# Performance work log

Hardware: AMD Instinct MI355X
Metric: run time of the kernel (lower is better)

## Reference

```python
import jax, jax.numpy as jnp
import numpy as np

N = 50000
E = 1600000
IN = 128
HID = 128
OUT = 64
NEG_SLOPE = 0.2  # DGL GATConv default leaky_relu slope


def _gat_layer(h, src, dst, W, al, ar, b, res=None, act=True):
    """DGL GATConv layer on an edge-list graph.
    h: [N, F_in]; W: [F_in, H*D]; al, ar, b: [H, D]; res: None | [N,H,D].
    Returns [N, H, D].
    """
    H, D = al.shape
    f = (h @ W).reshape(N, H, D)                      # fc projection
    el = jnp.sum(f * al, axis=-1)                     # [N, H]
    er = jnp.sum(f * ar, axis=-1)                     # [N, H]
    e = jax.nn.leaky_relu(el[src] + er[dst], NEG_SLOPE)  # [E, H]
    # edge softmax over incoming edges of each dst node
    m = jax.ops.segment_max(e, dst, num_segments=N)   # [N, H]
    ex = jnp.exp(e - m[dst])                          # [E, H]
    s = jax.ops.segment_sum(ex, dst, num_segments=N)  # [N, H]
    alpha = ex / s[dst]                               # [E, H]
    msg = f[src] * alpha[..., None]                   # [E, H, D]
    rst = jax.ops.segment_sum(msg, dst, num_segments=N)  # [N, H, D]
    if res is not None:
        rst = rst + res
    rst = rst + b                                     # bias [H, D] broadcast
    if act:
        rst = jax.nn.elu(rst)
    return rst


def setup_inputs() -> dict:
    key = jax.random.key(0)
    ks = jax.random.split(key, 16)
    x = jax.random.normal(ks[0], (N, IN), dtype=jnp.float32)
    src = jax.random.randint(ks[1], (E,), 0, N)
    dst = jax.random.randint(ks[2], (E,), 0, N)
    sc = 0.05
    # layer 0: IN -> 8 heads x 16, no residual, elu
    W0 = jax.random.normal(ks[3], (IN, 8 * 16), dtype=jnp.float32) * sc
    al0 = jax.random.normal(ks[4], (8, 16), dtype=jnp.float32) * sc
    ar0 = jax.random.normal(ks[5], (8, 16), dtype=jnp.float32) * sc
    b0 = jnp.zeros((8, 16), dtype=jnp.float32)
    # layer 1: HID -> 8 heads x 16, identity residual (HID == 8*16), elu
    W1 = jax.random.normal(ks[6], (HID, 8 * 16), dtype=jnp.float32) * sc
    al1 = jax.random.normal(ks[7], (8, 16), dtype=jnp.float32) * sc
    ar1 = jax.random.normal(ks[8], (8, 16), dtype=jnp.float32) * sc
    b1 = jnp.zeros((8, 16), dtype=jnp.float32)
    # layer 2: HID -> 1 head x 64, linear residual (128 != 64), no act
    W2 = jax.random.normal(ks[9], (HID, 1 * OUT), dtype=jnp.float32) * sc
    al2 = jax.random.normal(ks[10], (1, OUT), dtype=jnp.float32) * sc
    ar2 = jax.random.normal(ks[11], (1, OUT), dtype=jnp.float32) * sc
    b2 = jnp.zeros((1, OUT), dtype=jnp.float32)
    resW2 = jax.random.normal(ks[12], (HID, 1 * OUT), dtype=jnp.float32) * sc
    return {"x": x, "src": src, "dst": dst,
            "W0": W0, "al0": al0, "ar0": ar0, "b0": b0,
            "W1": W1, "al1": al1, "ar1": ar1, "b1": b1,
            "W2": W2, "al2": al2, "ar2": ar2, "b2": b2,
            "resW2": resW2}


def reference(x, src, dst, W0, al0, ar0, b0, W1, al1, ar1, b1,
              W2, al2, ar2, b2, resW2):
    # layer 0: no residual, elu, flatten heads (dropout=0)
    h = _gat_layer(x, src, dst, W0, al0, ar0, b0, res=None, act=True)
    h = h.reshape(N, -1)  # [N, 128]
    # layer 1: identity residual, elu, flatten heads
    res1 = h.reshape(N, 8, 16)
    h = _gat_layer(h, src, dst, W1, al1, ar1, b1, res=res1, act=True)
    h = h.reshape(N, -1)  # [N, 128]
    # layer 2: linear residual, no activation, mean over heads
    res2 = (h @ resW2).reshape(N, 1, OUT)
    h = _gat_layer(h, src, dst, W2, al2, ar2, b2, res=res2, act=False)
    return h.mean(axis=1)  # [N, 64]
```

## Files before the change

kernel.cpp:

```cpp
#include <hip/hip_runtime.h>
#include <hip/hip_fp16.h>
#include <math.h>


#define GN 50000
#define GE 1600000
#define NB 391
#define NBLK_A 512
#define CHUNK 3125
#define NBD 200
#define DCH 250

typedef _Float16 half8 __attribute__((ext_vector_type(8)));
typedef _Float16 half4v __attribute__((ext_vector_type(4)));
typedef float f32x4 __attribute__((ext_vector_type(4)));


__global__ __launch_bounds__(256) void bucketA(const int* __restrict__ dst, int* __restrict__ cnt) {
    __shared__ int hist[NB];
    for (int i = threadIdx.x; i < NB; i += 256) hist[i] = 0;
    __syncthreads();
    int b = blockIdx.x;
    int beg = b * CHUNK, end = beg + CHUNK;
    for (int i = beg + threadIdx.x; i < end; i += 256)
        atomicAdd(&hist[dst[i] >> 7], 1);
    __syncthreads();
    for (int k = threadIdx.x; k < NB; k += 256)
        cnt[k * NBLK_A + b] = hist[k];
}

__global__ __launch_bounds__(512) void bucketB(int* __restrict__ cnt, int* __restrict__ tot) {
    __shared__ int s[512];
    int k = blockIdx.x, t = threadIdx.x;
    int* row = cnt + k * NBLK_A;
    s[t] = row[t];
    __syncthreads();
    for (int ofs = 1; ofs < 512; ofs <<= 1) {
        int v = (t >= ofs) ? s[t - ofs] : 0;
        __syncthreads();
        s[t] += v;
        __syncthreads();
    }
    row[t] = (t == 0) ? 0 : s[t - 1];
    if (t == 511) tot[k] = s[511];
}

__global__ __launch_bounds__(512) void bucketB2(const int* __restrict__ tot, int* __restrict__ base,
                                                int* __restrict__ offs) {
    __shared__ int s[512];
    int t = threadIdx.x;
    s[t] = (t < NB) ? tot[t] : 0;
    __syncthreads();
    for (int ofs = 1; ofs < 512; ofs <<= 1) {
        int v = (t >= ofs) ? s[t - ofs] : 0;
        __syncthreads();
        s[t] += v;
        __syncthreads();
    }
    if (t <= NB) base[t] = (t == 0) ? 0 : s[t - 1];
    if (t == 0) offs[GN] = GE;
}

__global__ __launch_bounds__(256) void bucketC(const int* __restrict__ src, const int* __restrict__ dst,
                                               const int* __restrict__ cnt, const int* __restrict__ base,
                                               unsigned* __restrict__ ebuf) {
    __shared__ int cur[NB];
    int b = blockIdx.x;
    for (int k = threadIdx.x; k < NB; k += 256)
        cur[k] = base[k] + cnt[k * NBLK_A + b];
    __syncthreads();
    int beg = b * CHUNK, end = beg + CHUNK;
    for (int i = beg + threadIdx.x; i < end; i += 256) {
        int d = dst[i];
        int pos = atomicAdd(&cur[d >> 7], 1);
        ebuf[pos] = (unsigned)src[i] | ((unsigned)(d & 127) << 16);
    }
}

__global__ __launch_bounds__(256) void bucketD(const unsigned* __restrict__ ebuf, const int* __restrict__ base,
                                               int* __restrict__ offs, unsigned short* __restrict__ csrc) {
    __shared__ int hist[4096];
    __shared__ int psum[256];
    int k = blockIdx.x, t = threadIdx.x;
    #pragma unroll
    for (int i = 0; i < 16; ++i) hist[t * 16 + i] = 0;
    __syncthreads();
    int lo = base[k], hi = base[k + 1];
    for (int i = lo + t; i < hi; i += 256) {
        unsigned v = ebuf[i];
        unsigned key = ((v >> 16) << 5) | ((v & 0xFFFFu) >> 11);
        atomicAdd(&hist[key], 1);
    }
    __syncthreads();
    int loc[16];
    int s = 0;
    #pragma unroll
    for (int i = 0; i < 16; ++i) { loc[i] = s; s += hist[t * 16 + i]; }
    psum[t] = s;
    __syncthreads();
    for (int ofs = 1; ofs < 256; ofs <<= 1) {
        int v = (t >= ofs) ? psum[t - ofs] : 0;
        __syncthreads();
        psum[t] += v;
        __syncthreads();
    }
    int basek = lo + ((t == 0) ? 0 : psum[t - 1]);
    #pragma unroll
    for (int i = 0; i < 16; ++i) hist[t * 16 + i] = basek + loc[i];
    __syncthreads();
    if (t < 128) {
        int node = (k << 7) + t;
        if (node < GN) offs[node] = hist[t * 32];
    }
    __syncthreads();
    for (int i = lo + t; i < hi; i += 256) {
        unsigned v = ebuf[i];
        unsigned key = ((v >> 16) << 5) | ((v & 0xFFFFu) >> 11);
        int pos = atomicAdd(&hist[key], 1);
        csrc[pos] = (unsigned short)(v & 0xFFFFu);
    }
}


__global__ __launch_bounds__(256) void dhist(const int* __restrict__ offs, int* __restrict__ dcnt) {
    __shared__ int hist[128];
    int b = blockIdx.x, t = threadIdx.x;
    if (t < 128) hist[t] = 0;
    __syncthreads();
    int n = b * DCH + t;
    if (t < DCH && n < GN) {
        int d = offs[n + 1] - offs[n];
        d = (d > 127) ? 127 : d;
        atomicAdd(&hist[d], 1);
    }
    __syncthreads();
    if (t < 128) dcnt[t * NBD + b] = hist[t];
}

__global__ __launch_bounds__(256) void dscanB(int* __restrict__ dcnt, int* __restrict__ dtot) {
    __shared__ int s[256];
    int k = blockIdx.x, t = threadIdx.x;
    int* row = dcnt + k * NBD;
    s[t] = (t < NBD) ? row[t] : 0;
    __syncthreads();
    for (int ofs = 1; ofs < 256; ofs <<= 1) {
        int v = (t >= ofs) ? s[t - ofs] : 0;
        __syncthreads();
        s[t] += v;
        __syncthreads();
    }
    if (t < NBD) row[t] = (t == 0) ? 0 : s[t - 1];
    if (t == 255) dtot[k] = s[255];
}

__global__ __launch_bounds__(128) void dscanB2(const int* __restrict__ dtot, int* __restrict__ dbase) {
    __shared__ int s[128];
    int t = threadIdx.x;
    s[t] = dtot[t];
    __syncthreads();
    for (int ofs = 1; ofs < 128; ofs <<= 1) {
        int v = (t >= ofs) ? s[t - ofs] : 0;
        __syncthreads();
        s[t] += v;
        __syncthreads();
    }
    dbase[t] = (t == 0) ? 0 : s[t - 1];
}

__global__ __launch_bounds__(256) void dscat(const int* __restrict__ offs, const int* __restrict__ dcnt,
                                             const int* __restrict__ dbase, int* __restrict__ perm) {
    __shared__ int cur[128];
    int b = blockIdx.x, t = threadIdx.x;
    if (t < 128) cur[t] = dbase[t] + dcnt[t * NBD + b];
    __syncthreads();
    int n = b * DCH + t;
    if (t < DCH && n < GN) {
        int d = offs[n + 1] - offs[n];
        d = (d > 127) ? 127 : d;
        int pos = atomicAdd(&cur[d], 1);
        perm[pos] = n;
    }
}


__global__ __launch_bounds__(256) void prep(const float* __restrict__ W0, const float* __restrict__ W1,
                                            const float* __restrict__ W2, const float* __restrict__ rW2,
                                            const float* __restrict__ al0, const float* __restrict__ ar0,
                                            const float* __restrict__ al1, const float* __restrict__ ar1,
                                            const float* __restrict__ al2, const float* __restrict__ ar2,
                                            _Float16* __restrict__ w0t, _Float16* __restrict__ w1t,
                                            _Float16* __restrict__ w2t, _Float16* __restrict__ rw2t,
                                            _Float16* __restrict__ aB0, _Float16* __restrict__ aB1,
                                            _Float16* __restrict__ aB2) {
    int i = blockIdx.x * 256 + threadIdx.x;
    if (i < 16384) {
        int n = i >> 7, k = i & 127;
        w0t[i] = (_Float16)W0[k * 128 + n];
        w1t[i] = (_Float16)W1[k * 128 + n];
    }
    if (i < 8192) {
        int n = i >> 7, k = i & 127;
        w2t[i] = (_Float16)W2[k * 64 + n];
        rw2t[i] = (_Float16)rW2[k * 64 + n];
    }
    if (i < 2048) {
        int n = i >> 7, k = i & 127;
        _Float16 v0 = (_Float16)0.f, v1 = (_Float16)0.f, v2 = (_Float16)0.f;
        if (n < 8) {
            if ((k >> 4) == n) {
                v0 = (_Float16)al0[n * 16 + (k & 15)];
                v1 = (_Float16)al1[n * 16 + (k & 15)];
            }
        } else {
            int h = n - 8;
            if ((k >> 4) == h) {
                v0 = (_Float16)ar0[h * 16 + (k & 15)];
                v1 = (_Float16)ar1[h * 16 + (k & 15)];
            }
        }
        if (n == 0 && k < 64) v2 = (_Float16)al2[k];
        if (n == 1 && k < 64) v2 = (_Float16)ar2[k];
        aB0[i] = v0; aB1[i] = v1; aB2[i] = v2;
    }
}


template <int NT, bool AF32, bool DUAL, bool MULTI>
__global__ __launch_bounds__(256) void gemm_att(const void* __restrict__ Av,
                                                const _Float16* __restrict__ WT,
                                                const _Float16* __restrict__ WT2,
                                                const _Float16* __restrict__ attB,
                                                _Float16* __restrict__ C, _Float16* __restrict__ C2,
                                                float* __restrict__ elb, float* __restrict__ erb,
                                                int nrows) {
    const int N = NT * 16;
    __shared__ _Float16 lt[4][16][NT * 16 + 4];
    int wave = threadIdx.x >> 6, lane = threadIdx.x & 63;
    int quad = lane >> 4, l16 = lane & 15;
    int m = blockIdx.x * 64 + wave * 16 + l16;
    int mc = (m < nrows) ? m : (nrows - 1);
    half8 a[4];
    if (AF32) {
        const float* ap = (const float*)Av + (size_t)mc * 128 + quad * 8;
        #pragma unroll
        for (int kk = 0; kk < 4; ++kk) {
            float4 u = *(const float4*)(ap + kk * 32);
            float4 v = *(const float4*)(ap + kk * 32 + 4);
            half8 t;
            t[0] = (_Float16)u.x; t[1] = (_Float16)u.y; t[2] = (_Float16)u.z; t[3] = (_Float16)u.w;
            t[4] = (_Float16)v.x; t[5] = (_Float16)v.y; t[6] = (_Float16)v.z; t[7] = (_Float16)v.w;
            a[kk] = t;
        }
    } else {
        const _Float16* ap = (const _Float16*)Av + (size_t)mc * 128 + quad * 8;
        #pragma unroll
        for (int kk = 0; kk < 4; ++kk) a[kk] = *(const half8*)(ap + kk * 32);
    }
    f32x4 acc[NT];
    f32x4 acc2[DUAL ? NT : 1];
    #pragma unroll
    for (int nt = 0; nt < NT; ++nt) acc[nt] = (f32x4){0.f, 0.f, 0.f, 0.f};
    if (DUAL) {
        #pragma unroll
        for (int nt = 0; nt < NT; ++nt) acc2[nt] = (f32x4){0.f, 0.f, 0.f, 0.f};
    }
    const _Float16* wp = WT + (size_t)l16 * 128 + quad * 8;
    const _Float16* wp2 = DUAL ? (WT2 + (size_t)l16 * 128 + quad * 8) : WT;
    #pragma unroll
    for (int nt = 0; nt < NT; ++nt) {
        #pragma unroll
        for (int kk = 0; kk < 4; ++kk) {
            half8 b = *(const half8*)(wp + nt * 16 * 128 + kk * 32);
            acc[nt] = __builtin_amdgcn_mfma_f32_16x16x32_f16(a[kk], b, acc[nt], 0, 0, 0);
            if (DUAL) {
                half8 b2 = *(const half8*)(wp2 + nt * 16 * 128 + kk * 32);
                acc2[nt] = __builtin_amdgcn_mfma_f32_16x16x32_f16(a[kk], b2, acc2[nt], 0, 0, 0);
            }
        }
    }
    int row0 = blockIdx.x * 64 + wave * 16 + quad * 4;
    #pragma unroll
    for (int nt = 0; nt < NT; ++nt) {
        #pragma unroll
        for (int r = 0; r < 4; ++r) {
            _Float16 hv = (_Float16)acc[nt][r];
            lt[wave][quad * 4 + r][nt * 16 + l16] = hv;
            int row = row0 + r;
            if (row < nrows) {
                C[(size_t)row * N + nt * 16 + l16] = hv;
                if (DUAL) C2[(size_t)row * N + nt * 16 + l16] = (_Float16)acc2[nt][r];
            }
        }
    }
    f32x4 att = {0.f, 0.f, 0.f, 0.f};
    const _Float16* bp = attB + (size_t)l16 * 128 + quad * 8;
    constexpr int KCH = (NT == 8) ? 4 : 2;
    #pragma unroll
    for (int kk = 0; kk < KCH; ++kk) {
        const _Float16* lp = &lt[wave][l16][kk * 32 + quad * 8];
        half4v lo = *(const half4v*)lp;
        half4v hi = *(const half4v*)(lp + 4);
        half8 af = __builtin_shufflevector(lo, hi, 0, 1, 2, 3, 4, 5, 6, 7);
        half8 bf = *(const half8*)(bp + kk * 32);
        att = __builtin_amdgcn_mfma_f32_16x16x32_f16(af, bf, att, 0, 0, 0);
    }
    if (MULTI) {
        int hh = l16 & 7;
        float* dstp = (l16 < 8) ? elb : erb;
        #pragma unroll
        for (int r = 0; r < 4; ++r) {
            int row = row0 + r;
            if (row < nrows) dstp[row * 8 + hh] = att[r];
        }
    } else {
        if (l16 < 2) {
            float* dstp = (l16 == 0) ? elb : erb;
            #pragma unroll
            for (int r = 0; r < 4; ++r) {
                int row = row0 + r;
                if (row < nrows) dstp[row] = att[r];
            }
        }
    }
}


__global__ __launch_bounds__(256) void agg_multi(const int* __restrict__ offs,
                                                 const unsigned short* __restrict__ csrc,
                                                 const int* __restrict__ perm,
                                                 const _Float16* __restrict__ fh, const float* __restrict__ el,
                                                 const float* __restrict__ er, const float* __restrict__ bias,
                                                 const _Float16* __restrict__ resid, _Float16* __restrict__ out,
                                                 int n) {
    int slot = blockIdx.x * 16 + (threadIdx.x >> 4);
    int lg = threadIdx.x & 15;
    if (slot >= n) return;
    int node = perm[n - 1 - slot];
    int head = lg >> 1;
    float ern = er[node * 8 + head];
    int beg = offs[node], end = offs[node + 1];
    float acc[8] = {};
    float ssum = 0.f;
    int e = beg;
    for (; e + 4 <= end; e += 4) {
        int s0 = csrc[e], s1 = csrc[e + 1], s2 = csrc[e + 2], s3 = csrc[e + 3];
        float e0 = el[s0 * 8 + head] + ern;
        float e1 = el[s1 * 8 + head] + ern;
        float e2 = el[s2 * 8 + head] + ern;
        float e3 = el[s3 * 8 + head] + ern;
        half8 q0 = *(const half8*)(fh + (size_t)s0 * 128 + lg * 8);
        half8 q1 = *(const half8*)(fh + (size_t)s1 * 128 + lg * 8);
        half8 q2 = *(const half8*)(fh + (size_t)s2 * 128 + lg * 8);
        half8 q3 = *(const half8*)(fh + (size_t)s3 * 128 + lg * 8);
        e0 = fmaxf(e0, 0.2f * e0);
        e1 = fmaxf(e1, 0.2f * e1);
        e2 = fmaxf(e2, 0.2f * e2);
        e3 = fmaxf(e3, 0.2f * e3);
        float w0 = __expf(e0), w1 = __expf(e1), w2 = __expf(e2), w3 = __expf(e3);
        ssum += (w0 + w1) + (w2 + w3);
        #pragma unroll
        for (int i = 0; i < 8; ++i)
            acc[i] += w0 * (float)q0[i] + w1 * (float)q1[i]
                    + w2 * (float)q2[i] + w3 * (float)q3[i];
    }
    for (; e < end; ++e) {
        int s = csrc[e];
        float ev = el[s * 8 + head] + ern;
        ev = fmaxf(ev, 0.2f * ev);
        float w = __expf(ev);
        half8 q = *(const half8*)(fh + (size_t)s * 128 + lg * 8);
        ssum += w;
        #pragma unroll
        for (int i = 0; i < 8; ++i) acc[i] += w * (float)q[i];
    }
    float inv = (ssum > 0.f) ? 1.0f / ssum : 0.f;
    float o[8];
    #pragma unroll
    for (int j = 0; j < 8; ++j) o[j] = acc[j] * inv + bias[lg * 8 + j];
    if (resid) {
        half8 r = *(const half8*)(resid + (size_t)node * 128 + lg * 8);
        #pragma unroll
        for (int j = 0; j < 8; ++j) o[j] += (float)r[j];
    }
    half8 ov;
    #pragma unroll
    for (int j = 0; j < 8; ++j) {
        float v = o[j];
        v = (v > 0.f) ? v : expm1f(v);
        ov[j] = (_Float16)v;
    }
    *(half8*)(out + (size_t)node * 128 + lg * 8) = ov;
}

__global__ __launch_bounds__(256) void agg_single(const int* __restrict__ offs,
                                                  const unsigned short* __restrict__ csrc,
                                                  const int* __restrict__ perm,
                                                  const _Float16* __restrict__ fh, const float* __restrict__ el,
                                                  const float* __restrict__ er, const float* __restrict__ bias,
                                                  const _Float16* __restrict__ resid, float* __restrict__ out,
                                                  int n) {
    int slot = blockIdx.x * 16 + (threadIdx.x >> 4);
    int lg = threadIdx.x & 15;
    if (slot >= n) return;
    int node = perm[n - 1 - slot];
    float ern = er[node];
    int beg = offs[node], end = offs[node + 1];
    float acc[4] = {};
    float ssum = 0.f;
    int e = beg;
    for (; e + 4 <= end; e += 4) {
        int s0 = csrc[e], s1 = csrc[e + 1], s2 = csrc[e + 2], s3 = csrc[e + 3];
        float e0 = el[s0] + ern;
        float e1 = el[s1] + ern;
        float e2 = el[s2] + ern;
        float e3 = el[s3] + ern;
        half4v q0 = *(const half4v*)(fh + (size_t)s0 * 64 + lg * 4);
        half4v q1 = *(const half4v*)(fh + (size_t)s1 * 64 + lg * 4);
        half4v q2 = *(const half4v*)(fh + (size_t)s2 * 64 + lg * 4);
        half4v q3 = *(const half4v*)(fh + (size_t)s3 * 64 + lg * 4);
        e0 = fmaxf(e0, 0.2f * e0);
        e1 = fmaxf(e1, 0.2f * e1);
        e2 = fmaxf(e2, 0.2f * e2);
        e3 = fmaxf(e3, 0.2f * e3);
        float w0 = __expf(e0), w1 = __expf(e1), w2 = __expf(e2), w3 = __expf(e3);
        ssum += (w0 + w1) + (w2 + w3);
        #pragma unroll
        for (int i = 0; i < 4; ++i)
            acc[i] += w0 * (float)q0[i] + w1 * (float)q1[i]
                    + w2 * (float)q2[i] + w3 * (float)q3[i];
    }
    for (; e < end; ++e) {
        int s = csrc[e];
        float ev = el[s] + ern;
        ev = fmaxf(ev, 0.2f * ev);
        float w = __expf(ev);
        half4v q = *(const half4v*)(fh + (size_t)s * 64 + lg * 4);
        ssum += w;
        #pragma unroll
        for (int i = 0; i < 4; ++i) acc[i] += w * (float)q[i];
    }
    float inv = (ssum > 0.f) ? 1.0f / ssum : 0.f;
    half4v r = *(const half4v*)(resid + (size_t)node * 64 + lg * 4);
    float4 o;
    o.x = acc[0] * inv + bias[lg * 4 + 0] + (float)r[0];
    o.y = acc[1] * inv + bias[lg * 4 + 1] + (float)r[1];
    o.z = acc[2] * inv + bias[lg * 4 + 2] + (float)r[2];
    o.w = acc[3] * inv + bias[lg * 4 + 3] + (float)r[3];
    *(float4*)(out + (size_t)node * 64 + lg * 4) = o;
}


extern "C" void kernel_launch(void* const* d_in, const int* in_sizes, int n_in,
                              void* d_out, int out_size, void* d_ws, size_t ws_size,
                              hipStream_t stream) {
    const float* x     = (const float*)d_in[0];
    const int*   src   = (const int*)d_in[1];
    const int*   dst   = (const int*)d_in[2];
    const float* W0    = (const float*)d_in[3];
    const float* al0   = (const float*)d_in[4];
    const float* ar0   = (const float*)d_in[5];
    const float* b0    = (const float*)d_in[6];
    const float* W1    = (const float*)d_in[7];
    const float* al1   = (const float*)d_in[8];
    const float* ar1   = (const float*)d_in[9];
    const float* b1    = (const float*)d_in[10];
    const float* W2    = (const float*)d_in[11];
    const float* al2   = (const float*)d_in[12];
    const float* ar2   = (const float*)d_in[13];
    const float* b2    = (const float*)d_in[14];
    const float* resW2 = (const float*)d_in[15];
    float* out = (float*)d_out;

    char* w = (char*)d_ws;
    auto alloc = [&](size_t bytes) {
        char* p = w;
        w += (bytes + 255) & ~(size_t)255;
        return p;
    };
    int*            base  = (int*)alloc((size_t)(NB + 1) * 4);
    int*            offs  = (int*)alloc((size_t)(GN + 1) * 4);
    unsigned short* csrc  = (unsigned short*)alloc((size_t)GE * 2);
    int*            perm  = (int*)alloc((size_t)GN * 4);
    int*            dcnt  = (int*)alloc((size_t)128 * NBD * 4);
    int*            dtot  = (int*)alloc(128 * 4);
    int*            dbase = (int*)alloc(128 * 4);
    _Float16*       fbuf  = (_Float16*)alloc((size_t)GN * 128 * 2);
    float*          elb   = (float*)alloc((size_t)GN * 8 * 4);
    float*          erb   = (float*)alloc((size_t)GN * 8 * 4);
    _Float16*       hA    = (_Float16*)alloc((size_t)GN * 128 * 2);
    _Float16*       hB    = (_Float16*)alloc((size_t)GN * 128 * 2);
    _Float16*       res2  = (_Float16*)alloc((size_t)GN * 64 * 2);
    _Float16*       w0t   = (_Float16*)alloc(128 * 128 * 2);
    _Float16*       w1t   = (_Float16*)alloc(128 * 128 * 2);
    _Float16*       w2t   = (_Float16*)alloc(64 * 128 * 2);
    _Float16*       rw2t  = (_Float16*)alloc(64 * 128 * 2);
    _Float16*       aB0   = (_Float16*)alloc(16 * 128 * 2);
    _Float16*       aB1   = (_Float16*)alloc(16 * 128 * 2);
    _Float16*       aB2   = (_Float16*)alloc(16 * 128 * 2);

    int*      cnt  = (int*)hA;
    int*      tot  = (int*)hA + NB * NBLK_A;
    unsigned* ebuf = (unsigned*)hB;

    bucketA<<<NBLK_A, 256, 0, stream>>>(dst, cnt);
    bucketB<<<NB, 512, 0, stream>>>(cnt, tot);
    bucketB2<<<1, 512, 0, stream>>>(tot, base, offs);
    bucketC<<<NBLK_A, 256, 0, stream>>>(src, dst, cnt, base, ebuf);
    bucketD<<<NB, 256, 0, stream>>>(ebuf, base, offs, csrc);

    dhist<<<NBD, 256, 0, stream>>>(offs, dcnt);
    dscanB<<<128, 256, 0, stream>>>(dcnt, dtot);
    dscanB2<<<1, 128, 0, stream>>>(dtot, dbase);
    dscat<<<NBD, 256, 0, stream>>>(offs, dcnt, dbase, perm);

    prep<<<64, 256, 0, stream>>>(W0, W1, W2, resW2, al0, ar0, al1, ar1, al2, ar2,
                                 w0t, w1t, w2t, rw2t, aB0, aB1, aB2);

    dim3 gblk(256);
    int gemmGrid = (GN + 63) / 64;
    int aggGrid = (GN + 15) / 16;

    gemm_att<8, true, false, true><<<gemmGrid, gblk, 0, stream>>>(
        x, w0t, nullptr, aB0, fbuf, nullptr, elb, erb, GN);
    agg_multi<<<aggGrid, gblk, 0, stream>>>(offs, csrc, perm, fbuf, elb, erb, b0, nullptr, hA, GN);

    gemm_att<8, false, false, true><<<gemmGrid, gblk, 0, stream>>>(
        hA, w1t, nullptr, aB1, fbuf, nullptr, elb, erb, GN);
    agg_multi<<<aggGrid, gblk, 0, stream>>>(offs, csrc, perm, fbuf, elb, erb, b1, hA, hB, GN);

    gemm_att<4, false, true, false><<<gemmGrid, gblk, 0, stream>>>(
        hB, w2t, rw2t, aB2, fbuf, res2, elb, erb, GN);
    agg_single<<<aggGrid, gblk, 0, stream>>>(offs, csrc, perm, fbuf, elb, erb, b2, res2, out, GN);
}
```

Before: 358.6 us.

## Fuse degree histogram into CSR build and store attention logits in fp16

Computes the per-node degree histogram inside bucketD with global atomics, replacing the dhist/dscanB/dscanB2 chain. The small scan is merged into the weight-prep kernel, and the scatter now uses global atomics. The el/er attention logits are stored as fp16 instead of fp32, halving their footprint for the gather in the aggregation kernels. This cuts several launches and some memory traffic, at the cost of global atomic contention on 128 counters and reduced precision in the logits.

```diff
diff --git a/kernel.cpp b/kernel.cpp
--- a/kernel.cpp
+++ b/kernel.cpp
@@ -8,15 +8,15 @@
 #define NB 391
 #define NBLK_A 512
 #define CHUNK 3125
-#define NBD 200
-#define DCH 250
 
 typedef _Float16 half8 __attribute__((ext_vector_type(8)));
 typedef _Float16 half4v __attribute__((ext_vector_type(4)));
 typedef float f32x4 __attribute__((ext_vector_type(4)));
 
 
-__global__ __launch_bounds__(256) void bucketA(const int* __restrict__ dst, int* __restrict__ cnt) {
+__global__ __launch_bounds__(256) void bucketA(const int* __restrict__ dst, int* __restrict__ cnt,
+                                               int* __restrict__ gdcnt) {
+    if (blockIdx.x == 0 && threadIdx.x < 128) gdcnt[threadIdx.x] = 0;
     __shared__ int hist[NB];
     for (int i = threadIdx.x; i < NB; i += 256) hist[i] = 0;
     __syncthreads();
@@ -78,7 +78,8 @@
 }
 
 __global__ __launch_bounds__(256) void bucketD(const unsigned* __restrict__ ebuf, const int* __restrict__ base,
-                                               int* __restrict__ offs, unsigned short* __restrict__ csrc) {
+                                               int* __restrict__ offs, unsigned short* __restrict__ csrc,
+                                               int* __restrict__ gdcnt) {
     __shared__ int hist[4096];
     __shared__ int psum[256];
     int k = blockIdx.x, t = threadIdx.x;
@@ -110,7 +111,14 @@
     __syncthreads();
     if (t < 128) {
         int node = (k << 7) + t;
-        if (node < GN) offs[node] = hist[t * 32];
+        if (node < GN) {
+            int st = hist[t * 32];
+            offs[node] = st;
+            int en = (t < 127) ? hist[(t + 1) * 32] : hi;
+            int d = en - st;
+            d = (d > 127) ? 127 : d;
+            atomicAdd(&gdcnt[d], 1);
+        }
     }
     __syncthreads();
     for (int i = lo + t; i < hi; i += 256) {
@@ -122,78 +130,33 @@
 }
 
 
-__global__ __launch_bounds__(256) void dhist(const int* __restrict__ offs, int* __restrict__ dcnt) {
-    __shared__ int hist[128];
-    int b = blockIdx.x, t = threadIdx.x;
-    if (t < 128) hist[t] = 0;
-    __syncthreads();
-    int n = b * DCH + t;
-    if (t < DCH && n < GN) {
-        int d = offs[n + 1] - offs[n];
-        d = (d > 127) ? 127 : d;
-        atomicAdd(&hist[d], 1);
-    }
-    __syncthreads();
-    if (t < 128) dcnt[t * NBD + b] = hist[t];
-}
-
-__global__ __launch_bounds__(256) void dscanB(int* __restrict__ dcnt, int* __restrict__ dtot) {
-    __shared__ int s[256];
-    int k = blockIdx.x, t = threadIdx.x;
-    int* row = dcnt + k * NBD;
-    s[t] = (t < NBD) ? row[t] : 0;
-    __syncthreads();
-    for (int ofs = 1; ofs < 256; ofs <<= 1) {
-        int v = (t >= ofs) ? s[t - ofs] : 0;
-        __syncthreads();
-        s[t] += v;
-        __syncthreads();
-    }
-    if (t < NBD) row[t] = (t == 0) ? 0 : s[t - 1];
-    if (t == 255) dtot[k] = s[255];
-}
-
-__global__ __launch_bounds__(128) void dscanB2(const int* __restrict__ dtot, int* __restrict__ dbase) {
-    __shared__ int s[128];
-    int t = threadIdx.x;
-    s[t] = dtot[t];
-    __syncthreads();
-    for (int ofs = 1; ofs < 128; ofs <<= 1) {
-        int v = (t >= ofs) ? s[t - ofs] : 0;
-        __syncthreads();
-        s[t] += v;
-        __syncthreads();
-    }
-    dbase[t] = (t == 0) ? 0 : s[t - 1];
-}
-
-__global__ __launch_bounds__(256) void dscat(const int* __restrict__ offs, const int* __restrict__ dcnt,
-                                             const int* __restrict__ dbase, int* __restrict__ perm) {
-    __shared__ int cur[128];
-    int b = blockIdx.x, t = threadIdx.x;
-    if (t < 128) cur[t] = dbase[t] + dcnt[t * NBD + b];
-    __syncthreads();
-    int n = b * DCH + t;
-    if (t < DCH && n < GN) {
-        int d = offs[n + 1] - offs[n];
-        d = (d > 127) ? 127 : d;
-        int pos = atomicAdd(&cur[d], 1);
-        perm[pos] = n;
-    }
-}
-
-
-__global__ __launch_bounds__(256) void prep(const float* __restrict__ W0, const float* __restrict__ W1,
-                                            const float* __restrict__ W2, const float* __restrict__ rW2,
-                                            const float* __restrict__ al0, const float* __restrict__ ar0,
-                                            const float* __restrict__ al1, const float* __restrict__ ar1,
-                                            const float* __restrict__ al2, const float* __restrict__ ar2,
-                                            _Float16* __restrict__ w0t, _Float16* __restrict__ w1t,
-                                            _Float16* __restrict__ w2t, _Float16* __restrict__ rw2t,
-                                            _Float16* __restrict__ aB0, _Float16* __restrict__ aB1,
-                                            _Float16* __restrict__ aB2) {
-    int i = blockIdx.x * 256 + threadIdx.x;
-    if (i < 16384) {
+__global__ __launch_bounds__(256) void dscan_prep(const int* __restrict__ gdcnt, int* __restrict__ gcur,
+                                                  const float* __restrict__ W0, const float* __restrict__ W1,
+                                                  const float* __restrict__ W2, const float* __restrict__ rW2,
+                                                  const float* __restrict__ al0, const float* __restrict__ ar0,
+                                                  const float* __restrict__ al1, const float* __restrict__ ar1,
+                                                  const float* __restrict__ al2, const float* __restrict__ ar2,
+                                                  _Float16* __restrict__ w0t, _Float16* __restrict__ w1t,
+                                                  _Float16* __restrict__ w2t, _Float16* __restrict__ rw2t,
+                                                  _Float16* __restrict__ aB0, _Float16* __restrict__ aB1,
+                                                  _Float16* __restrict__ aB2) {
+    if (blockIdx.x == 0) {
+        __shared__ int s[128];
+        int t = threadIdx.x;
+        if (t < 128) s[t] = gdcnt[t];
+        __syncthreads();
+        for (int ofs = 1; ofs < 128; ofs <<= 1) {
+            int v = 0;
+            if (t < 128 && t >= ofs) v = s[t - ofs];
+            __syncthreads();
+            if (t < 128) s[t] += v;
+            __syncthreads();
+        }
+        if (t < 128) gcur[t] = (t == 0) ? 0 : s[t - 1];
+        return;
+    }
+    int i = (blockIdx.x - 1) * 256 + threadIdx.x;
+    {
         int n = i >> 7, k = i & 127;
         w0t[i] = (_Float16)W0[k * 128 + n];
         w1t[i] = (_Float16)W1[k * 128 + n];
@@ -224,6 +187,16 @@
     }
 }
 
+__global__ __launch_bounds__(256) void dscat(const int* __restrict__ offs, int* __restrict__ gcur,
+                                             int* __restrict__ perm) {
+    int n = blockIdx.x * 256 + threadIdx.x;
+    if (n >= GN) return;
+    int d = offs[n + 1] - offs[n];
+    d = (d > 127) ? 127 : d;
+    int pos = atomicAdd(&gcur[d], 1);
+    perm[pos] = n;
+}
+
 
 template <int NT, bool AF32, bool DUAL, bool MULTI>
 __global__ __launch_bounds__(256) void gemm_att(const void* __restrict__ Av,
@@ -231,7 +204,7 @@
                                                 const _Float16* __restrict__ WT2,
                                                 const _Float16* __restrict__ attB,
                                                 _Float16* __restrict__ C, _Float16* __restrict__ C2,
-                                                float* __restrict__ elb, float* __restrict__ erb,
+                                                _Float16* __restrict__ elb, _Float16* __restrict__ erb,
                                                 int nrows) {
     const int N = NT * 16;
     __shared__ _Float16 lt[4][16][NT * 16 + 4];
@@ -306,19 +279,19 @@
     }
     if (MULTI) {
         int hh = l16 & 7;
-        float* dstp = (l16 < 8) ? elb : erb;
+        _Float16* dstp = (l16 < 8) ? elb : erb;
         #pragma unroll
         for (int r = 0; r < 4; ++r) {
             int row = row0 + r;
-            if (row < nrows) dstp[row * 8 + hh] = att[r];
+            if (row < nrows) dstp[row * 8 + hh] = (_Float16)att[r];
         }
     } else {
         if (l16 < 2) {
-            float* dstp = (l16 == 0) ? elb : erb;
+            _Float16* dstp = (l16 == 0) ? elb : erb;
             #pragma unroll
             for (int r = 0; r < 4; ++r) {
                 int row = row0 + r;
-                if (row < nrows) dstp[row] = att[r];
+                if (row < nrows) dstp[row] = (_Float16)att[r];
             }
         }
     }
@@ -328,8 +301,10 @@
 __global__ __launch_bounds__(256) void agg_multi(const int* __restrict__ offs,
                                                  const unsigned short* __restrict__ csrc,
                                                  const int* __restrict__ perm,
-                                                 const _Float16* __restrict__ fh, const float* __restrict__ el,
-                                                 const float* __restrict__ er, const float* __restrict__ bias,
+                                                 const _Float16* __restrict__ fh,
+                                                 const _Float16* __restrict__ el,
+                                                 const _Float16* __restrict__ er,
+                                                 const float* __restrict__ bias,
                                                  const _Float16* __restrict__ resid, _Float16* __restrict__ out,
                                                  int n) {
     int slot = blockIdx.x * 16 + (threadIdx.x >> 4);
@@ -337,17 +312,17 @@
     if (slot >= n) return;
     int node = perm[n - 1 - slot];
     int head = lg >> 1;
-    float ern = er[node * 8 + head];
+    float ern = (float)er[node * 8 + head];
     int beg = offs[node], end = offs[node + 1];
     float acc[8] = {};
     float ssum = 0.f;
     int e = beg;
     for (; e + 4 <= end; e += 4) {
         int s0 = csrc[e], s1 = csrc[e + 1], s2 = csrc[e + 2], s3 = csrc[e + 3];
-        float e0 = el[s0 * 8 + head] + ern;
-        float e1 = el[s1 * 8 + head] + ern;
-        float e2 = el[s2 * 8 + head] + ern;
-        float e3 = el[s3 * 8 + head] + ern;
+        float e0 = (float)el[s0 * 8 + head] + ern;
+        float e1 = (float)el[s1 * 8 + head] + ern;
+        float e2 = (float)el[s2 * 8 + head] + ern;
+        float e3 = (float)el[s3 * 8 + head] + ern;
         half8 q0 = *(const half8*)(fh + (size_t)s0 * 128 + lg * 8);
         half8 q1 = *(const half8*)(fh + (size_t)s1 * 128 + lg * 8);
         half8 q2 = *(const half8*)(fh + (size_t)s2 * 128 + lg * 8);
@@ -365,7 +340,7 @@
     }
     for (; e < end; ++e) {
         int s = csrc[e];
-        float ev = el[s * 8 + head] + ern;
+        float ev = (float)el[s * 8 + head] + ern;
         ev = fmaxf(ev, 0.2f * ev);
         float w = __expf(ev);
         half8 q = *(const half8*)(fh + (size_t)s * 128 + lg * 8);
@@ -395,25 +370,27 @@
 __global__ __launch_bounds__(256) void agg_single(const int* __restrict__ offs,
                                                   const unsigned short* __restrict__ csrc,
                                                   const int* __restrict__ perm,
-                                                  const _Float16* __restrict__ fh, const float* __restrict__ el,
-                                                  const float* __restrict__ er, const float* __restrict__ bias,
+                                                  const _Float16* __restrict__ fh,
+                                                  const _Float16* __restrict__ el,
+                                                  const _Float16* __restrict__ er,
+                                                  const float* __restrict__ bias,
                                                   const _Float16* __restrict__ resid, float* __restrict__ out,
                                                   int n) {
     int slot = blockIdx.x * 16 + (threadIdx.x >> 4);
     int lg = threadIdx.x & 15;
     if (slot >= n) return;
     int node = perm[n - 1 - slot];
-    float ern = er[node];
+    float ern = (float)er[node];
     int beg = offs[node], end = offs[node + 1];
     float acc[4] = {};
     float ssum = 0.f;
     int e = beg;
     for (; e + 4 <= end; e += 4) {
         int s0 = csrc[e], s1 = csrc[e + 1], s2 = csrc[e + 2], s3 = csrc[e + 3];
-        float e0 = el[s0] + ern;
-        float e1 = el[s1] + ern;
-        float e2 = el[s2] + ern;
-        float e3 = el[s3] + ern;
+        float e0 = (float)el[s0] + ern;
+        float e1 = (float)el[s1] + ern;
+        float e2 = (float)el[s2] + ern;
+        float e3 = (float)el[s3] + ern;
         half4v q0 = *(const half4v*)(fh + (size_t)s0 * 64 + lg * 4);
         half4v q1 = *(const half4v*)(fh + (size_t)s1 * 64 + lg * 4);
         half4v q2 = *(const half4v*)(fh + (size_t)s2 * 64 + lg * 4);
@@ -431,7 +408,7 @@
     }
     for (; e < end; ++e) {
         int s = csrc[e];
-        float ev = el[s] + ern;
+        float ev = (float)el[s] + ern;
         ev = fmaxf(ev, 0.2f * ev);
         float w = __expf(ev);
         half4v q = *(const half4v*)(fh + (size_t)s * 64 + lg * 4);
@@ -481,12 +458,11 @@
     int*            offs  = (int*)alloc((size_t)(GN + 1) * 4);
     unsigned short* csrc  = (unsigned short*)alloc((size_t)GE * 2);
     int*            perm  = (int*)alloc((size_t)GN * 4);
-    int*            dcnt  = (int*)alloc((size_t)128 * NBD * 4);
-    int*            dtot  = (int*)alloc(128 * 4);
-    int*            dbase = (int*)alloc(128 * 4);
+    int*            gdcnt = (int*)alloc(128 * 4);
+    int*            gcur  = (int*)alloc(128 * 4);
     _Float16*       fbuf  = (_Float16*)alloc((size_t)GN * 128 * 2);
-    float*          elb   = (float*)alloc((size_t)GN * 8 * 4);
-    float*          erb   = (float*)alloc((size_t)GN * 8 * 4);
+    _Float16*       elb   = (_Float16*)alloc((size_t)GN * 8 * 2);
+    _Float16*       erb   = (_Float16*)alloc((size_t)GN * 8 * 2);
     _Float16*       hA    = (_Float16*)alloc((size_t)GN * 128 * 2);
     _Float16*       hB    = (_Float16*)alloc((size_t)GN * 128 * 2);
     _Float16*       res2  = (_Float16*)alloc((size_t)GN * 64 * 2);
@@ -502,19 +478,16 @@
     int*      tot  = (int*)hA + NB * NBLK_A;
     unsigned* ebuf = (unsigned*)hB;
 
-    bucketA<<<NBLK_A, 256, 0, stream>>>(dst, cnt);
+    bucketA<<<NBLK_A, 256, 0, stream>>>(dst, cnt, gdcnt);
     bucketB<<<NB, 512, 0, stream>>>(cnt, tot);
     bucketB2<<<1, 512, 0, stream>>>(tot, base, offs);
     bucketC<<<NBLK_A, 256, 0, stream>>>(src, dst, cnt, base, ebuf);
-    bucketD<<<NB, 256, 0, stream>>>(ebuf, base, offs, csrc);
-
-    dhist<<<NBD, 256, 0, stream>>>(offs, dcnt);
-    dscanB<<<128, 256, 0, stream>>>(dcnt, dtot);
-    dscanB2<<<1, 128, 0, stream>>>(dtot, dbase);
-    dscat<<<NBD, 256, 0, stream>>>(offs, dcnt, dbase, perm);
-
-    prep<<<64, 256, 0, stream>>>(W0, W1, W2, resW2, al0, ar0, al1, ar1, al2, ar2,
-                                 w0t, w1t, w2t, rw2t, aB0, aB1, aB2);
+    bucketD<<<NB, 256, 0, stream>>>(ebuf, base, offs, csrc, gdcnt);
+
+    dscan_prep<<<65, 256, 0, stream>>>(gdcnt, gcur, W0, W1, W2, resW2,
+                                       al0, ar0, al1, ar1, al2, ar2,
+                                       w0t, w1t, w2t, rw2t, aB0, aB1, aB2);
+    dscat<<<(GN + 255) / 256, 256, 0, stream>>>(offs, gcur, perm);
 
     dim3 gblk(256);
     int gemmGrid = (GN + 63) / 64;
```

After: 513.7 us. 43.3% more time.
